# Kernel optimization log

Measured on AMD Instinct MI355X. Metric: run time of the kernel, lower is better.

The kernel has to match this reference:

```python
import jax, jax.numpy as jnp
import numpy as np

DT = 0.01            # init_kwargs dt
P1, P2, PA = 1.0, 0.1, 0.01   # reward penalties from __init__
TERM_SCALE = 10.0    # truncated terminal reward scale


def setup_inputs() -> dict:
    key = jax.random.key(0)
    k1, k2, k3, k4 = jax.random.split(key, 4)
    B = 65536
    initial_states = jax.random.normal(k1, (B, 2), dtype=jnp.float32)
    b_param = jax.random.normal(k2, (B, 1), dtype=jnp.float32)
    # simple linear state-feedback controller parameters (stand-in for `controller`)
    W = jax.random.normal(k3, (2, 1), dtype=jnp.float32) * 0.1
    bias = jax.random.normal(k4, (1,), dtype=jnp.float32) * 0.1
    return {"initial_states": initial_states, "b_param": b_param, "W": W, "bias": bias, "num_steps": 512}


def _rollout(initial_states, b_param, W, bias, num_steps):
    b_val = b_param[:, 0:1]          # [B,1]
    sin_b = jnp.sin(b_val)           # constant over episode

    def dyn(s, u):
        # x1_dot = x2 ; x2_dot = x1 + b*u + sin(b)
        x1, x2 = s[:, 0:1], s[:, 1:2]
        return jnp.concatenate([x2, x1 + b_val * u + sin_b], axis=1)

    def step(carry, _):
        state, total = carry
        u = state @ W + bias          # controller action [B,1], held fixed over RK4 stages
        k1 = dyn(state, u)
        k2 = dyn(state + 0.5 * DT * k1, u)
        k3 = dyn(state + 0.5 * DT * k2, u)
        k4 = dyn(state + DT * k3, u)
        ns = state + (DT / 6.0) * (k1 + 2 * k2 + 2 * k3 + k4)
        r = -(P1 * ns[:, 0:1] ** 2 + P2 * ns[:, 1:2] ** 2 + PA * u ** 2) * DT
        return (ns, total + r), None

    total0 = jnp.zeros((initial_states.shape[0], 1), dtype=initial_states.dtype)
    (final_state, total), _ = jax.lax.scan(step, (initial_states, total0), None, length=num_steps)
    # truncated terminal penalty (TARGET_STATE == 0)
    total = total - (P1 * final_state[:, 0:1] ** 2 + P2 * final_state[:, 1:2] ** 2) * TERM_SCALE
    return total


def reference(initial_states, b_param, W, bias, num_steps):
    return _rollout(initial_states, b_param, W, bias, num_steps)
```

## Files before the change

### kernel.cpp

```cpp
#include <hip/hip_runtime.h>


#define DT_F 0.01f
#define P1_F 1.0f
#define P2_F 0.1f
#define PA_F 0.01f
#define TERM_SCALE_F 10.0f

__device__ __forceinline__ void rk4_step(float x1, float x2, float c,
                                         float& nx, float& ny) {
    const float h  = DT_F;
    const float hh = 0.5f * DT_F;
    const float h6 = DT_F / 6.0f;
    float k1x = x2;
    float k1y = x1 + c;
    float a2x = fmaf(hh, k1x, x1);
    float a2y = fmaf(hh, k1y, x2);
    float k2x = a2y;
    float k2y = a2x + c;
    float a3x = fmaf(hh, k2x, x1);
    float a3y = fmaf(hh, k2y, x2);
    float k3x = a3y;
    float k3y = a3x + c;
    float a4x = fmaf(h, k3x, x1);
    float a4y = fmaf(h, k3y, x2);
    float k4x = a4y;
    float k4y = a4x + c;
    nx = fmaf(h6, k1x + 2.0f * k2x + 2.0f * k3x + k4x, x1);
    ny = fmaf(h6, k1y + 2.0f * k2y + 2.0f * k3y + k4y, x2);
}

__global__ __launch_bounds__(256) void nct_rollout_kernel(
    const float* __restrict__ s0,
    const float* __restrict__ bparam,
    const float* __restrict__ W,
    const float* __restrict__ bias,
    const int* __restrict__ nsteps_p,
    float* __restrict__ out,
    int B) {
    int i = blockIdx.x * blockDim.x + threadIdx.x;
    if (i >= B) return;

    const float w0 = W[0];
    const float w1 = W[1];
    const float bs = bias[0];
    const int nsteps = nsteps_p[0];

    float2 s = reinterpret_cast<const float2*>(s0)[i];
    float x1 = s.x;
    float x2 = s.y;
    const float b = bparam[i];
    const float sinb = sinf(b);

    const float alpha = b * w0;
    const float beta  = b * w1;
    const float gamma = fmaf(b, bs, sinb);

    float a00, a10, a01, a11, d0, d1;
    rk4_step(1.0f, 0.0f, alpha, a00, a10);
    rk4_step(0.0f, 1.0f, beta,  a01, a11);
    rk4_step(0.0f, 0.0f, gamma, d0,  d1);

    float accX = 0.0f;
    float accY = 0.0f;
    float accU = 0.0f;
    #pragma unroll 4
    for (int t = 0; t < nsteps; ++t) {
        float u  = fmaf(w0, x1, fmaf(w1, x2, bs));
        float nx = fmaf(a00, x1, fmaf(a01, x2, d0));
        float ny = fmaf(a10, x1, fmaf(a11, x2, d1));
        accX = fmaf(nx, nx, accX);
        accY = fmaf(ny, ny, accY);
        accU = fmaf(u, u, accU);
        x1 = nx;
        x2 = ny;
    }

    float total = -DT_F * (P1_F * accX + P2_F * accY + PA_F * accU)
                  - TERM_SCALE_F * (fmaf(P1_F * x1, x1, P2_F * x2 * x2));
    out[i] = total;
}

extern "C" void kernel_launch(void* const* d_in, const int* in_sizes, int n_in,
                              void* d_out, int out_size, void* d_ws, size_t ws_size,
                              hipStream_t stream) {
    const float* s0     = (const float*)d_in[0];
    const float* bparam = (const float*)d_in[1];
    const float* W      = (const float*)d_in[2];
    const float* bias   = (const float*)d_in[3];
    const int*   nsteps = (const int*)d_in[4];
    float* out = (float*)d_out;
    const int B = in_sizes[1];

    dim3 block(256);
    dim3 grid((B + 255) / 256);
    nct_rollout_kernel<<<grid, block, 0, stream>>>(s0, bparam, W, bias, nsteps,
                                                   out, B);
}
```

Before: 69.36 us.

## Replace sequential affine rollout with binary-doubling quadratic-form accumulation

Replaces the per-step loop over num_steps with repeated squaring of the affine step map, carrying the accumulated quadratic cost matrix alongside it so the whole rollout costs O(log n) matrix operations. The final reward is evaluated as a quadratic form in the initial state. This removes the serial dependency chain of 512 iterations per thread, at the cost of more arithmetic per doubling step and possibly different floating-point rounding.

```diff
diff --git a/kernel.cpp b/kernel.cpp
--- a/kernel.cpp
+++ b/kernel.cpp
@@ -30,7 +30,38 @@
     ny = fmaf(h6, k1y + 2.0f * k2y + 2.0f * k3y + k4y, x2);
 }
 
-__global__ __launch_bounds__(256) void nct_rollout_kernel(
+__device__ __forceinline__ void congr(
+    float s00, float s01, float s02, float s11, float s12, float s22,
+    float a00, float a01, float a10, float a11, float d0, float d1,
+    float& r00, float& r01, float& r02, float& r11, float& r12, float& r22) {
+    float M00 = fmaf(s00, a00, s01 * a10);
+    float M01 = fmaf(s00, a01, s01 * a11);
+    float M02 = fmaf(s00, d0, fmaf(s01, d1, s02));
+    float M10 = fmaf(s01, a00, s11 * a10);
+    float M11 = fmaf(s01, a01, s11 * a11);
+    float M12 = fmaf(s01, d0, fmaf(s11, d1, s12));
+    float M22 = fmaf(s02, d0, fmaf(s12, d1, s22));
+    r00 = fmaf(a00, M00, a10 * M10);
+    r01 = fmaf(a00, M01, a10 * M11);
+    r02 = fmaf(a00, M02, a10 * M12);
+    r11 = fmaf(a01, M01, a11 * M11);
+    r12 = fmaf(a01, M02, a11 * M12);
+    r22 = fmaf(d0, M02, fmaf(d1, M12, M22));
+}
+
+__device__ __forceinline__ void compose(
+    float b00, float b01, float b10, float b11, float bd0, float bd1,
+    float a00, float a01, float a10, float a11, float ad0, float ad1,
+    float& c00, float& c01, float& c10, float& c11, float& cd0, float& cd1) {
+    c00 = fmaf(b00, a00, b01 * a10);
+    c01 = fmaf(b00, a01, b01 * a11);
+    c10 = fmaf(b10, a00, b11 * a10);
+    c11 = fmaf(b10, a01, b11 * a11);
+    cd0 = fmaf(b00, ad0, fmaf(b01, ad1, bd0));
+    cd1 = fmaf(b10, ad0, fmaf(b11, ad1, bd1));
+}
+
+__global__ __launch_bounds__(256) void nct_doubling_kernel(
     const float* __restrict__ s0,
     const float* __restrict__ bparam,
     const float* __restrict__ W,
@@ -44,41 +75,76 @@
     const float w0 = W[0];
     const float w1 = W[1];
     const float bs = bias[0];
-    const int nsteps = nsteps_p[0];
+    unsigned n = (unsigned)nsteps_p[0];
 
     float2 s = reinterpret_cast<const float2*>(s0)[i];
-    float x1 = s.x;
-    float x2 = s.y;
-    const float b = bparam[i];
-    const float sinb = sinf(b);
+    const float x1 = s.x;
+    const float x2 = s.y;
+    const float bp = bparam[i];
+    const float sinb = sinf(bp);
 
-    const float alpha = b * w0;
-    const float beta  = b * w1;
-    const float gamma = fmaf(b, bs, sinb);
+    const float alpha = bp * w0;
+    const float beta  = bp * w1;
+    const float gamma = fmaf(bp, bs, sinb);
 
-    float a00, a10, a01, a11, d0, d1;
-    rk4_step(1.0f, 0.0f, alpha, a00, a10);
-    rk4_step(0.0f, 1.0f, beta,  a01, a11);
-    rk4_step(0.0f, 0.0f, gamma, d0,  d1);
+    float t00, t10, t01, t11, td0, td1;
+    rk4_step(1.0f, 0.0f, alpha, t00, t10);
+    rk4_step(0.0f, 1.0f, beta,  t01, t11);
+    rk4_step(0.0f, 0.0f, gamma, td0, td1);
 
-    float accX = 0.0f;
-    float accY = 0.0f;
-    float accU = 0.0f;
-    #pragma unroll 4
-    for (int t = 0; t < nsteps; ++t) {
-        float u  = fmaf(w0, x1, fmaf(w1, x2, bs));
-        float nx = fmaf(a00, x1, fmaf(a01, x2, d0));
-        float ny = fmaf(a10, x1, fmaf(a11, x2, d1));
-        accX = fmaf(nx, nx, accX);
-        accY = fmaf(ny, ny, accY);
-        accU = fmaf(u, u, accU);
-        x1 = nx;
-        x2 = ny;
+    float Sb00 = DT_F * fmaf(P1_F * t00, t00, fmaf(P2_F * t10, t10, PA_F * w0 * w0));
+    float Sb01 = DT_F * fmaf(P1_F * t00, t01, fmaf(P2_F * t10, t11, PA_F * w0 * w1));
+    float Sb02 = DT_F * fmaf(P1_F * t00, td0, fmaf(P2_F * t10, td1, PA_F * w0 * bs));
+    float Sb11 = DT_F * fmaf(P1_F * t01, t01, fmaf(P2_F * t11, t11, PA_F * w1 * w1));
+    float Sb12 = DT_F * fmaf(P1_F * t01, td0, fmaf(P2_F * t11, td1, PA_F * w1 * bs));
+    float Sb22 = DT_F * fmaf(P1_F * td0, td0, fmaf(P2_F * td1, td1, PA_F * bs * bs));
+    float b00 = t00, b01 = t01, b10 = t10, b11 = t11, bd0 = td0, bd1 = td1;
+
+    float Sr00 = 0.f, Sr01 = 0.f, Sr02 = 0.f, Sr11 = 0.f, Sr12 = 0.f, Sr22 = 0.f;
+    float r00 = 1.f, r01 = 0.f, r10 = 0.f, r11 = 1.f, rd0 = 0.f, rd1 = 0.f;
+
+    while (n) {
+        if (n & 1u) {
+            float q00, q01, q02, q11, q12, q22;
+            congr(Sb00, Sb01, Sb02, Sb11, Sb12, Sb22,
+                  r00, r01, r10, r11, rd0, rd1,
+                  q00, q01, q02, q11, q12, q22);
+            Sr00 += q00; Sr01 += q01; Sr02 += q02;
+            Sr11 += q11; Sr12 += q12; Sr22 += q22;
+            float n00, n01, n10, n11, nd0, nd1;
+            compose(b00, b01, b10, b11, bd0, bd1,
+                    r00, r01, r10, r11, rd0, rd1,
+                    n00, n01, n10, n11, nd0, nd1);
+            r00 = n00; r01 = n01; r10 = n10; r11 = n11; rd0 = nd0; rd1 = nd1;
+        }
+        n >>= 1u;
+        if (n) {
+            float q00, q01, q02, q11, q12, q22;
+            congr(Sb00, Sb01, Sb02, Sb11, Sb12, Sb22,
+                  b00, b01, b10, b11, bd0, bd1,
+                  q00, q01, q02, q11, q12, q22);
+            Sb00 += q00; Sb01 += q01; Sb02 += q02;
+            Sb11 += q11; Sb12 += q12; Sb22 += q22;
+            float n00, n01, n10, n11, nd0, nd1;
+            compose(b00, b01, b10, b11, bd0, bd1,
+                    b00, b01, b10, b11, bd0, bd1,
+                    n00, n01, n10, n11, nd0, nd1);
+            b00 = n00; b01 = n01; b10 = n10; b11 = n11; bd0 = nd0; bd1 = nd1;
+        }
     }
 
-    float total = -DT_F * (P1_F * accX + P2_F * accY + PA_F * accU)
-                  - TERM_SCALE_F * (fmaf(P1_F * x1, x1, P2_F * x2 * x2));
-    out[i] = total;
+    float G00 = fmaf(TERM_SCALE_F, fmaf(P1_F * r00, r00, P2_F * r10 * r10), Sr00);
+    float G01 = fmaf(TERM_SCALE_F, fmaf(P1_F * r00, r01, P2_F * r10 * r11), Sr01);
+    float G02 = fmaf(TERM_SCALE_F, fmaf(P1_F * r00, rd0, P2_F * r10 * rd1), Sr02);
+    float G11 = fmaf(TERM_SCALE_F, fmaf(P1_F * r01, r01, P2_F * r11 * r11), Sr11);
+    float G12 = fmaf(TERM_SCALE_F, fmaf(P1_F * r01, rd0, P2_F * r11 * rd1), Sr12);
+    float G22 = fmaf(TERM_SCALE_F, fmaf(P1_F * rd0, rd0, P2_F * rd1 * rd1), Sr22);
+
+    float q = fmaf(G00 * x1, x1,
+              fmaf(2.0f * x1, fmaf(G01, x2, G02),
+              fmaf(G11 * x2, x2,
+              fmaf(2.0f * G12, x2, G22))));
+    out[i] = -q;
 }
 
 extern "C" void kernel_launch(void* const* d_in, const int* in_sizes, int n_in,
@@ -94,6 +160,6 @@
 
     dim3 block(256);
     dim3 grid((B + 255) / 256);
-    nct_rollout_kernel<<<grid, block, 0, stream>>>(s0, bparam, W, bias, nsteps,
-                                                   out, B);
+    nct_doubling_kernel<<<grid, block, 0, stream>>>(s0, bparam, W, bias, nsteps,
+                                                    out, B);
 }
```

Measured after the change: 63.07 us. 9.1% less time.
